# Performance work log

Hardware: AMD Instinct MI355X
Metric: run time of the kernel (lower is better)

## Reference

```python
import jax, jax.numpy as jnp
import numpy as np

NF, D, H, HD, NL, FF = 5, 64, 8, 8, 2, 128   # features, d_model, heads, head_dim, layers, ffn
NQ, QL, NC = 8, 3, 3                          # qubits, quantum layers, classes


def pos_encoding(S, d):
    pos = np.arange(S, dtype=np.float32)[:, None]
    div = np.exp(np.arange(0, d, 2, dtype=np.float32) * (-np.log(10000.0) / d))
    pe = np.zeros((S, d), np.float32)
    pe[:, 0::2] = np.sin(pos * div)
    pe[:, 1::2] = np.cos(pos * div)
    return jnp.asarray(pe)


def layernorm(x, g, b, eps=1e-5):
    m = x.mean(-1, keepdims=True)
    v = ((x - m) ** 2).mean(-1, keepdims=True)
    return (x - m) * jax.lax.rsqrt(v + eps) * g + b


def apply1q(psi, U, w):
    # psi: (2,)*NQ complex state; apply 2x2 gate U on wire w
    p = jnp.moveaxis(psi, w, 0)
    sh = p.shape
    p = (U @ p.reshape(2, -1)).reshape(sh)
    return jnp.moveaxis(p, 0, w)


def cnot(psi, c, t):
    p = jnp.moveaxis(psi, (c, t), (0, 1))
    sh = p.shape
    p = p.reshape(2, 2, -1)
    p = jnp.stack([p[0], p[1, ::-1]], 0).reshape(sh)  # flip target when control=1
    return jnp.moveaxis(p, (0, 1), (c, t))


def rx_mat(t):
    c, s = jnp.cos(t / 2), jnp.sin(t / 2)
    return jnp.stack([jnp.stack([c + 0j, -1j * s]), jnp.stack([-1j * s, c + 0j])]).astype(jnp.complex64)


def rot_mat(phi, th, om):
    # qml.Rot = RZ(om) RY(th) RZ(phi)
    c, s = jnp.cos(th / 2), jnp.sin(th / 2)
    return jnp.stack([
        jnp.stack([jnp.exp(-0.5j * (phi + om)) * c, -jnp.exp(0.5j * (phi - om)) * s]),
        jnp.stack([jnp.exp(-0.5j * (phi - om)) * s, jnp.exp(0.5j * (phi + om)) * c]),
    ]).astype(jnp.complex64)


def quantum_circuit(angles, weights):
    # angles: [NQ], weights: [QL, NQ, 3]. Circuit: QL x (AngleEmbedding(RX) + StronglyEntanglingLayer(range=1))
    psi = jnp.zeros((2,) * NQ, jnp.complex64).at[(0,) * NQ].set(1.0)
    for l in range(QL):
        for w in range(NQ):
            psi = apply1q(psi, rx_mat(angles[w]), w)
        for w in range(NQ):
            psi = apply1q(psi, rot_mat(weights[l, w, 0], weights[l, w, 1], weights[l, w, 2]), w)
        for w in range(NQ):
            psi = cnot(psi, w, (w + 1) % NQ)
    prob = jnp.abs(psi) ** 2
    zs = []
    for w in range(NC):  # <Z_w> = p(0_w) - p(1_w)
        marg = prob.sum(axis=tuple(i for i in range(NQ) if i != w))
        zs.append(marg[0] - marg[1])
    # von Neumann entropy of wires 0..3 (trace out wires 4..7), natural log
    mat = psi.reshape(16, 16)
    rho = mat @ mat.conj().T
    ev = jnp.clip(jnp.linalg.eigvalsh(rho), 1e-10, 1.0)
    ent = -jnp.sum(ev * jnp.log(ev))
    return jnp.stack(zs), ent


def setup_inputs() -> dict:
    key = jax.random.key(0)
    ks = jax.random.split(key, 30)
    sc = 0.02
    inp = {
        'x': jax.random.normal(ks[0], (16, 1024, NF), jnp.float32),
        'Wemb': sc * jax.random.normal(ks[1], (NF, D)), 'bemb': jnp.zeros((D,)),
        'Wq': sc * jax.random.normal(ks[2], (NL, D, D)), 'bq': jnp.zeros((NL, D)),
        'Wk': sc * jax.random.normal(ks[3], (NL, D, D)), 'bk': jnp.zeros((NL, D)),
        'Wv': sc * jax.random.normal(ks[4], (NL, D, D)), 'bv': jnp.zeros((NL, D)),
        'Wo': sc * jax.random.normal(ks[5], (NL, D, D)), 'bo': jnp.zeros((NL, D)),
        'ln1g': jnp.ones((NL, D)), 'ln1b': jnp.zeros((NL, D)),
        'ln2g': jnp.ones((NL, D)), 'ln2b': jnp.zeros((NL, D)),
        'Wf1': sc * jax.random.normal(ks[6], (NL, D, FF)), 'bf1': jnp.zeros((NL, FF)),
        'Wf2': sc * jax.random.normal(ks[7], (NL, FF, D)), 'bf2': jnp.zeros((NL, D)),
        'Wp1': sc * jax.random.normal(ks[8], (D, 32)), 'bp1': jnp.zeros((32,)),
        'Wp2': sc * jax.random.normal(ks[9], (32, NQ)), 'bp2': jnp.zeros((NQ,)),
        'qweights': jax.random.normal(ks[10], (QL, NQ, 3)),
    }
    return inp


def reference(x, Wemb, bemb, Wq, bq, Wk, bk, Wv, bv, Wo, bo, ln1g, ln1b, ln2g, ln2b,
              Wf1, bf1, Wf2, bf2, Wp1, bp1, Wp2, bp2, qweights):
    B, S, _ = x.shape
    h = x @ Wemb + bemb + pos_encoding(S, D)[None]  # aug + dropout are identity in eval
    scale = np.float32(1.0 / np.sqrt(HD))
    for l in range(NL):
        q = (h @ Wq[l] + bq[l]).reshape(B, S, H, HD).transpose(0, 2, 1, 3)
        k = (h @ Wk[l] + bk[l]).reshape(B, S, H, HD).transpose(0, 2, 1, 3)
        v = (h @ Wv[l] + bv[l]).reshape(B, S, H, HD).transpose(0, 2, 1, 3)
        att = jax.nn.softmax(jnp.einsum('bhsd,bhtd->bhst', q, k) * scale, axis=-1)
        o = jnp.einsum('bhst,bhtd->bhsd', att, v).transpose(0, 2, 1, 3).reshape(B, S, D)
        h = layernorm(h + o @ Wo[l] + bo[l], ln1g[l], ln1b[l])
        ff = jax.nn.relu(h @ Wf1[l] + bf1[l]) @ Wf2[l] + bf2[l]
        h = layernorm(h + ff, ln2g[l], ln2b[l])
    pooled = h.mean(1)
    feats = jax.nn.relu(pooled @ Wp1 + bp1) @ Wp2 + bp2
    angles = jnp.tanh(feats) * np.float32(np.pi)
    logits, ent = jax.vmap(quantum_circuit, in_axes=(0, None))(angles, qweights)
    return logits, ent
```

## Files before the change

### kernel.cpp

```cpp
#include <hip/hip_runtime.h>
#include <math.h>

#define BB 16
#define SS 1024
#define NF 5
#define DD 64
#define HH 8
#define HDIM 8
#define NLAYER 2
#define FFD 128
#define NQ 8
#define QLAY 3
#define NC 3
#define NSWEEP 5
#define BHS_TOT (BB * HH * SS)

typedef __fp16 hf2 __attribute__((ext_vector_type(2)));
typedef __fp16 h8  __attribute__((ext_vector_type(8)));
typedef float  f4x __attribute__((ext_vector_type(4)));

__device__ __forceinline__ int   f2i_(float x) { union { float f; int i; } u; u.f = x; return u.i; }
__device__ __forceinline__ float i2f_(int x)   { union { float f; int i; } u; u.i = x; return u.f; }

__device__ __forceinline__ float bperm_(int pa, float x) {
    return i2f_(__builtin_amdgcn_ds_bpermute(pa, f2i_(x)));
}

__device__ __forceinline__ float half32_(float x) {
#if defined(__has_builtin)
#if __has_builtin(__builtin_amdgcn_permlane32_swap)
    int xi = f2i_(x);
    auto r = __builtin_amdgcn_permlane32_swap(xi, xi, false, false);
    int r0 = (int)r[0], r1 = (int)r[1];
    return i2f_(r0 == xi ? r1 : r0);
#else
    return __shfl_xor(x, 32);
#endif
#else
    return __shfl_xor(x, 32);
#endif
}

template<int M> __device__ __forceinline__ float lx(float x) {
    if constexpr (M == 0) {
        return x;
    } else if constexpr (M == 1) {
        return i2f_(__builtin_amdgcn_update_dpp(0, f2i_(x), 0xB1, 0xF, 0xF, true));
    } else if constexpr (M == 2) {
        return i2f_(__builtin_amdgcn_update_dpp(0, f2i_(x), 0x4E, 0xF, 0xF, true));
    } else if constexpr (M == 3) {
        return i2f_(__builtin_amdgcn_update_dpp(0, f2i_(x), 0x1B, 0xF, 0xF, true));
    } else if constexpr (M < 32) {
        return i2f_(__builtin_amdgcn_ds_swizzle(f2i_(x), (M << 10) | 0x1F));
    } else {
        return lx<M & 31>(half32_(x));
    }
}

__global__ __launch_bounds__(64) void k_embed(const float* __restrict__ x,
                                              const float* __restrict__ Wemb,
                                              const float* __restrict__ bemb,
                                              float* __restrict__ h) {
    int bs = blockIdx.x;
    int s  = bs & (SS - 1);
    int d  = threadIdx.x;
    const float* xr = x + bs * NF;
    float acc = bemb[d];
#pragma unroll
    for (int f = 0; f < NF; ++f) acc += xr[f] * Wemb[f * DD + d];
    int i = d >> 1;
    float div = expf((float)(2 * i) * (-9.210340371976184f / 64.0f));
    float ang = (float)s * div;
    float pe = (d & 1) ? cosf(ang) : sinf(ang);
    h[bs * DD + d] = acc + pe;
}

__global__ __launch_bounds__(64) void k_qkv(const float* __restrict__ h,
                                            const float* __restrict__ Wq, const float* __restrict__ bq,
                                            const float* __restrict__ Wk, const float* __restrict__ bk,
                                            const float* __restrict__ Wv, const float* __restrict__ bv,
                                            hf2* __restrict__ qh, hf2* __restrict__ kh,
                                            hf2* __restrict__ vt, int l) {
    __shared__ float hrow[4][DD];
    int d   = threadIdx.x;
    int bs0 = blockIdx.x * 4;
#pragma unroll
    for (int r = 0; r < 4; ++r) hrow[r][d] = h[(bs0 + r) * DD + d];
    __syncthreads();
    const float* wq = Wq + l * DD * DD;
    const float* wk = Wk + l * DD * DD;
    const float* wv = Wv + l * DD * DD;
    float aq[4], ak[4], av[4];
    float bqv = bq[l * DD + d], bkv = bk[l * DD + d], bvv = bv[l * DD + d];
#pragma unroll
    for (int r = 0; r < 4; ++r) { aq[r] = bqv; ak[r] = bkv; av[r] = bvv; }
#pragma unroll 4
    for (int i = 0; i < DD; ++i) {
        float wqv = wq[i * DD + d], wkv = wk[i * DD + d], wvv = wv[i * DD + d];
#pragma unroll
        for (int r = 0; r < 4; ++r) {
            float hv = hrow[r][i];
            aq[r] += hv * wqv; ak[r] += hv * wkv; av[r] += hv * wvv;
        }
    }
    int hh = d >> 3, hd = d & 7;
    const float qs = 0.3535533906f;
    float aqp[4], akp[4];
#pragma unroll
    for (int r = 0; r < 4; ++r) { aqp[r] = __shfl_xor(aq[r], 1); akp[r] = __shfl_xor(ak[r], 1); }
    if ((hd & 1) == 0) {
#pragma unroll
        for (int r = 0; r < 4; ++r) {
            int bs = bs0 + r;
            int b = bs >> 10, s = bs & 1023;
            int bhs = ((b * HH + hh) << 10) | s;
            qh[bhs * 4 + (hd >> 1)] = __builtin_amdgcn_cvt_pkrtz(aq[r] * qs, aqp[r] * qs);
            kh[bhs * 4 + (hd >> 1)] = __builtin_amdgcn_cvt_pkrtz(ak[r], akp[r]);
        }
    }
    {
        int b = bs0 >> 10, s0 = bs0 & 1023;
        int vrow = (b * HH + hh) * 8 + hd;
        hf2* vp = vt + vrow * 512 + (s0 >> 1);
        vp[0] = __builtin_amdgcn_cvt_pkrtz(av[0], av[1]);
        vp[1] = __builtin_amdgcn_cvt_pkrtz(av[2], av[3]);
    }
}

__global__ __launch_bounds__(256) void k_attn(const float4* __restrict__ qh4,
                                              const float4* __restrict__ kh4,
                                              const float4* __restrict__ vt4,
                                              float* __restrict__ Ao) {
    int bh  = blockIdx.x;
    int sb  = blockIdx.y;
    int tid = threadIdx.x;
    int wv  = tid >> 6;
    int L   = tid & 63;
    int m = L & 15, quad = L >> 4;
    union U { float4 f; h8 h; };
    h8 hz = {0,0,0,0,0,0,0,0};
    h8 bQ = hz;
    if (quad == 0) { U u; u.f = qh4[(bh << 10) | (sb * 64 + wv * 16 + m)]; bQ = u.h; }
    int kmap = 8 * (m >> 2) + (m & 3);
    const float4* kbase = kh4 + (bh << 10);
    const float4* vbase = vt4 + ((bh * 8 + m) << 7);
    f4x Oacc = {0.f, 0.f, 0.f, 0.f};
    float ls = 0.f;
    for (int kc = 0; kc < 32; ++kc) {
        h8 aK0 = hz, aK1 = hz;
        if (quad == 0) {
            U u0, u1;
            u0.f = kbase[kc * 32 + kmap];
            u1.f = kbase[kc * 32 + kmap + 4];
            aK0 = u0.h; aK1 = u1.h;
        }
        f4x S0 = {0.f,0.f,0.f,0.f}, S1 = {0.f,0.f,0.f,0.f};
        S0 = __builtin_amdgcn_mfma_f32_16x16x32_f16(aK0, bQ, S0, 0, 0, 0);
        S1 = __builtin_amdgcn_mfma_f32_16x16x32_f16(aK1, bQ, S1, 0, 0, 0);
        float p0 = __expf(S0[0]), p1 = __expf(S0[1]);
        float p2 = __expf(S0[2]), p3 = __expf(S0[3]);
        float p4 = __expf(S1[0]), p5 = __expf(S1[1]);
        float p6 = __expf(S1[2]), p7 = __expf(S1[3]);
        ls += (p0 + p1 + p2 + p3) + (p4 + p5 + p6 + p7);
        hf2 c0 = __builtin_amdgcn_cvt_pkrtz(p0, p1);
        hf2 c1 = __builtin_amdgcn_cvt_pkrtz(p2, p3);
        hf2 c2 = __builtin_amdgcn_cvt_pkrtz(p4, p5);
        hf2 c3 = __builtin_amdgcn_cvt_pkrtz(p6, p7);
        h8 aP;
        aP[0] = c0[0]; aP[1] = c0[1]; aP[2] = c1[0]; aP[3] = c1[1];
        aP[4] = c2[0]; aP[5] = c2[1]; aP[6] = c3[0]; aP[7] = c3[1];
        h8 bV = hz;
        if (m < 8) {
            U uv; uv.f = vbase[kc * 4 + quad];
            bV = uv.h;
        }
        Oacc = __builtin_amdgcn_mfma_f32_16x16x32_f16(aP, bV, Oacc, 0, 0, 0);
    }
    ls += __shfl_xor(ls, 16);
    ls += __shfl_xor(ls, 32);
    float d0 = bperm_((4 * quad + 0) << 2, ls);
    float d1 = bperm_((4 * quad + 1) << 2, ls);
    float d2 = bperm_((4 * quad + 2) << 2, ls);
    float d3 = bperm_((4 * quad + 3) << 2, ls);
    if (m < 8) {
        int srow = sb * 64 + wv * 16 + quad * 4;
        int base = (((bh << 10) | srow) << 3) + m;
        Ao[base]      = Oacc[0] / d0;
        Ao[base + 8]  = Oacc[1] / d1;
        Ao[base + 16] = Oacc[2] / d2;
        Ao[base + 24] = Oacc[3] / d3;
    }
}

__global__ __launch_bounds__(128) void k_mid(const float* __restrict__ Ao,
                                             const float* __restrict__ Wo, const float* __restrict__ bo,
                                             const float* __restrict__ g1, const float* __restrict__ b1,
                                             const float* __restrict__ Wf1, const float* __restrict__ bf1,
                                             const float* __restrict__ Wf2, const float* __restrict__ bf2,
                                             const float* __restrict__ g2, const float* __restrict__ b2,
                                             float* __restrict__ h, int l) {
    __shared__ float orow[4][DD];
    __shared__ float h1s[4][DD];
    __shared__ float frow[4][FFD];
    int t    = threadIdx.x;
    int d    = t & 63;
    int half = t >> 6;
    int bs0  = blockIdx.x * 4;
    int hh = d >> 3, hd = d & 7;
    int r0 = half * 2, r1 = r0 + 1;

#pragma unroll
    for (int rr = 0; rr < 2; ++rr) {
        int r  = r0 + rr;
        int bs = bs0 + r;
        int b = bs >> 10, s = bs & 1023;
        int bhs = ((b * HH + hh) << 10) | s;
        orow[r][d] = Ao[(bhs << 3) + hd];
    }
    __syncthreads();

    {
        const float* w = Wo + l * DD * DD;
        float bias = bo[l * DD + d];
        float acc0 = bias, acc1 = bias;
#pragma unroll 4
        for (int i = 0; i < DD; ++i) {
            float wv = w[i * DD + d];
            acc0 += orow[r0][i] * wv;
            acc1 += orow[r1][i] * wv;
        }
        float gg = g1[l * DD + d], bb = b1[l * DD + d];
        float accs[2] = {acc0, acc1};
#pragma unroll
        for (int rr = 0; rr < 2; ++rr) {
            int r = r0 + rr;
            float a = accs[rr] + h[(bs0 + r) * DD + d];
            float sum = a;
            for (int off = 32; off; off >>= 1) sum += __shfl_xor(sum, off);
            float mean = sum * (1.f / 64.f);
            float dx = a - mean;
            float vs = dx * dx;
            for (int off = 32; off; off >>= 1) vs += __shfl_xor(vs, off);
            float rstd = rsqrtf(vs * (1.f / 64.f) + 1e-5f);
            h1s[r][d] = dx * rstd * gg + bb;
        }
    }
    __syncthreads();

    {
        const float* w = Wf1 + l * DD * FFD;
        float bv = bf1[l * FFD + t];
        float a0 = bv, a1 = bv, a2 = bv, a3 = bv;
#pragma unroll 4
        for (int i = 0; i < DD; ++i) {
            float wv = w[i * FFD + t];
            a0 += h1s[0][i]*wv; a1 += h1s[1][i]*wv;
            a2 += h1s[2][i]*wv; a3 += h1s[3][i]*wv;
        }
        frow[0][t] = fmaxf(a0, 0.f); frow[1][t] = fmaxf(a1, 0.f);
        frow[2][t] = fmaxf(a2, 0.f); frow[3][t] = fmaxf(a3, 0.f);
    }
    __syncthreads();

    {
        const float* w = Wf2 + l * FFD * DD;
        float bias = bf2[l * DD + d];
        float acc0 = bias, acc1 = bias;
#pragma unroll 4
        for (int i = 0; i < FFD; ++i) {
            float wv = w[i * DD + d];
            acc0 += frow[r0][i] * wv;
            acc1 += frow[r1][i] * wv;
        }
        float gg = g2[l * DD + d], bb = b2[l * DD + d];
        float accs[2] = {acc0, acc1};
#pragma unroll
        for (int rr = 0; rr < 2; ++rr) {
            int r = r0 + rr;
            float a = accs[rr] + h1s[r][d];
            float sum = a;
            for (int off = 32; off; off >>= 1) sum += __shfl_xor(sum, off);
            float mean = sum * (1.f / 64.f);
            float dx = a - mean;
            float vs = dx * dx;
            for (int off = 32; off; off >>= 1) vs += __shfl_xor(vs, off);
            float rstd = rsqrtf(vs * (1.f / 64.f) + 1e-5f);
            h[(bs0 + r) * DD + d] = dx * rstd * gg + bb;
        }
    }
}

__global__ __launch_bounds__(64) void k_pool(const float* __restrict__ h, float* __restrict__ pp) {
    int b = blockIdx.x, c = blockIdx.y, d = threadIdx.x;
    const float* hp = h + (b * SS + c * 128) * DD + d;
    float acc = 0.f;
#pragma unroll 8
    for (int s = 0; s < 128; ++s) acc += hp[s * DD];
    pp[(b * 8 + c) * DD + d] = acc;
}

__global__ __launch_bounds__(64) void k_tail(const float* __restrict__ pp,
                                             const float* __restrict__ Wp1, const float* __restrict__ bp1,
                                             const float* __restrict__ Wp2, const float* __restrict__ bp2,
                                             const float* __restrict__ qw,
                                             float* __restrict__ out) {
    __shared__ float pool_s[DD];
    __shared__ float hid[32];
    __shared__ float ang_s[NQ];
    __shared__ float ucoef[QLAY * 16][8];
    __shared__ float2 Ps2[256];
    int b = blockIdx.x; int L = threadIdx.x;
    int lb4 = L << 2;

    {
        float acc = 0.f;
#pragma unroll
        for (int c = 0; c < 8; ++c) acc += pp[(b * 8 + c) * DD + L];
        pool_s[L] = acc * (1.f / 1024.f);
    }
    __syncthreads();
    if (L < 32) {
        float a = bp1[L];
#pragma unroll 8
        for (int i = 0; i < DD; ++i) a += pool_s[i] * Wp1[i * 32 + L];
        hid[L] = fmaxf(a, 0.f);
    }
    __syncthreads();
    if (L < NQ) {
        float a = bp2[L];
#pragma unroll 8
        for (int j = 0; j < 32; ++j) a += hid[j] * Wp2[j * NQ + L];
        ang_s[L] = tanhf(a) * 3.14159265358979f;
    }
    __syncthreads();

    if (L < QLAY * 16) {
        int l = L >> 4, g8 = L & 15, w = g8 & 7;
        float u00r, u00i, u01r, u01i, u10r, u10i, u11r, u11i;
        if (g8 < 8) {
            float ha = 0.5f * ang_s[w];
            float c = __cosf(ha), s = __sinf(ha);
            u00r = c;   u00i = 0.f; u01r = 0.f; u01i = -s;
            u10r = 0.f; u10i = -s;  u11r = c;   u11i = 0.f;
        } else {
            const float* p3 = qw + (l * NQ + w) * 3;
            float phi = p3[0], th = p3[1], om = p3[2];
            float ct = __cosf(0.5f * th), st = __sinf(0.5f * th);
            float al = 0.5f * (phi + om), be = 0.5f * (phi - om);
            float ca = __cosf(al), sa = __sinf(al), cb = __cosf(be), sb = __sinf(be);
            u00r =  ct * ca; u00i = -ct * sa;
            u01r = -st * cb; u01i = -st * sb;
            u10r =  st * cb; u10i = -st * sb;
            u11r =  ct * ca; u11i =  ct * sa;
        }
        float* up = ucoef[L];
        up[0] = u00r; up[1] = u00i; up[2] = u01r; up[3] = u01i;
        up[4] = u10r; up[5] = u10i; up[6] = u11r; up[7] = u11i;
    }
    __syncthreads();

    float ar[4], ai[4];
#pragma unroll
    for (int r = 0; r < 4; ++r) { ar[r] = 0.f; ai[r] = 0.f; }
    if (L == 0) ar[0] = 1.f;

#pragma unroll 1
    for (int l = 0; l < QLAY; ++l) {
#pragma unroll 1
        for (int g8 = 0; g8 < 16; ++g8) {
            const float* up = ucoef[(l << 4) | g8];
            float u00r = up[0], u00i = up[1], u01r = up[2], u01i = up[3];
            float u10r = up[4], u10i = up[5], u11r = up[6], u11i = up[7];
            int p = 7 - (g8 & 7);
            if (p >= 6) {
#pragma unroll
                for (int pi_ = 0; pi_ < 2; ++pi_) {
                    int lo = (p == 7) ? pi_ : pi_ * 2;
                    int hi = (p == 7) ? pi_ + 2 : pi_ * 2 + 1;
                    float r0 = ar[lo], m0 = ai[lo], r1 = ar[hi], m1 = ai[hi];
                    ar[lo] = u00r*r0 - u00i*m0 + u01r*r1 - u01i*m1;
                    ai[lo] = u00r*m0 + u00i*r0 + u01r*m1 + u01i*r1;
                    ar[hi] = u10r*r0 - u10i*m0 + u11r*r1 - u11i*m1;
                    ai[hi] = u10r*m0 + u10i*r0 + u11r*m1 + u11i*r1;
                }
            } else {
                int pa  = lb4 ^ (4 << p);
                int bit = (L >> p) & 1;
                float car = bit ? u11r : u00r, cai = bit ? u11i : u00i;
                float cpr = bit ? u10r : u01r, cpi = bit ? u10i : u01i;
#pragma unroll
                for (int r = 0; r < 4; ++r) {
                    float pre = bperm_(pa, ar[r]);
                    float pim = bperm_(pa, ai[r]);
                    float nr = car*ar[r] - cai*ai[r] + cpr*pre - cpi*pim;
                    float ni = car*ai[r] + cai*ar[r] + cpr*pim + cpi*pre;
                    ar[r] = nr; ai[r] = ni;
                }
            }
        }
        { float t0=ar[2]; ar[2]=ar[3]; ar[3]=t0; t0=ai[2]; ai[2]=ai[3]; ai[3]=t0; }
        ar[1] = half32_(ar[1]); ai[1] = half32_(ai[1]);
        ar[3] = half32_(ar[3]); ai[3] = half32_(ai[3]);
#pragma unroll 1
        for (int w = 2; w <= 6; ++w) {
            int pc = 7 - w, pt = 6 - w;
            int pa = lb4 ^ (4 << pt);
            bool ctrl = (L >> pc) & 1;
#pragma unroll
            for (int r = 0; r < 4; ++r) {
                float swr = bperm_(pa, ar[r]);
                float swi = bperm_(pa, ai[r]);
                ar[r] = ctrl ? swr : ar[r];
                ai[r] = ctrl ? swi : ai[r];
            }
        }
        {
            bool ctrl = L & 1;
            float n0r = ctrl ? ar[2] : ar[0], n2r = ctrl ? ar[0] : ar[2];
            float n0i = ctrl ? ai[2] : ai[0], n2i = ctrl ? ai[0] : ai[2];
            float n1r = ctrl ? ar[3] : ar[1], n3r = ctrl ? ar[1] : ar[3];
            float n1i = ctrl ? ai[3] : ai[1], n3i = ctrl ? ai[1] : ai[3];
            ar[0]=n0r; ar[1]=n1r; ar[2]=n2r; ar[3]=n3r;
            ai[0]=n0i; ai[1]=n1i; ai[2]=n2i; ai[3]=n3i;
        }
    }

    {
        float p0 = ar[0]*ar[0]+ai[0]*ai[0];
        float p1 = ar[1]*ar[1]+ai[1]*ai[1];
        float p2 = ar[2]*ar[2]+ai[2]*ai[2];
        float p3 = ar[3]*ar[3]+ai[3]*ai[3];
        float z0 = p0 + p1 - p2 - p3;
        float z1 = p0 - p1 + p2 - p3;
        float zs = p0 + p1 + p2 + p3;
        float z2 = (L & 32) ? -zs : zs;
#pragma unroll 1
        for (int off = 1; off < 64; off <<= 1) {
            int pa = lb4 ^ (off << 2);
            z0 += bperm_(pa, z0);
            z1 += bperm_(pa, z1);
            z2 += bperm_(pa, z2);
        }
        if (L == 0) {
            out[b * NC + 0] = z0;
            out[b * NC + 1] = z1;
            out[b * NC + 2] = z2;
        }
    }

#pragma unroll
    for (int r = 0; r < 4; ++r) Ps2[(r << 6) | L] = make_float2(ar[r], ai[r]);
    __syncthreads();
    int c   = L >> 2;
    int seg = L & 3;
    float gr[4], gi[4];
#pragma unroll
    for (int j = 0; j < 4; ++j) {
        float2 t = Ps2[(seg * 4 + j) * 16 + c];
        gr[j] = t.x; gi[j] = t.y;
    }
    float alm = 0.f;
#pragma unroll
    for (int j = 0; j < 4; ++j) alm += gr[j]*gr[j] + gi[j]*gi[j];
    alm += lx<1>(alm);
    alm += lx<2>(alm);

#pragma unroll 1
    for (int sweep = 0; sweep < NSWEEP; ++sweep) {
#pragma unroll 1
        for (int m = 1; m <= 15; ++m) {
            int pa = lb4 ^ (m << 4);
            float pgr[4], pgi[4];
#pragma unroll
            for (int j = 0; j < 4; ++j) {
                pgr[j] = bperm_(pa, gr[j]);
                pgi[j] = bperm_(pa, gi[j]);
            }
            float bep = bperm_(pa, alm);
            float d = 0.f, e = 0.f;
#pragma unroll
            for (int j = 0; j < 4; ++j) {
                d += gr[j]*pgr[j] + gi[j]*pgi[j];
                e += gr[j]*pgi[j] - gi[j]*pgr[j];
            }
            d += lx<1>(d); e += lx<1>(e);
            d += lx<2>(d); e += lx<2>(e);
            float g2 = d*d + e*e;
            float cth = 1.f, sth = 0.f, cph = 1.f, sph = 0.f, gn = 0.f;
            if (g2 > 1e-26f) {
                gn = __builtin_amdgcn_sqrtf(g2);
                float ginv = __builtin_amdgcn_rcpf(gn);
                cph = d * ginv; sph = -e * ginv;
                float tau = (alm - bep) * (0.5f * ginv);
                float t = ((tau >= 0.f) ? 1.f : -1.f) *
                          __builtin_amdgcn_rcpf(fabsf(tau) + __builtin_amdgcn_sqrtf(1.f + tau*tau));
                cth = __builtin_amdgcn_rsqf(1.f + t*t);
                sth = t * cth;
            }
#pragma unroll
            for (int j = 0; j < 4; ++j) {
                float er = cph*pgr[j] - sph*pgi[j];
                float ei = cph*pgi[j] + sph*pgr[j];
                gr[j] = cth * gr[j] + sth * er;
                gi[j] = cth * gi[j] + sth * ei;
            }
            alm = cth*cth*alm + sth*sth*bep + 2.f*cth*sth*gn;
        }
    }

    float alm2 = 0.f;
#pragma unroll
    for (int j = 0; j < 4; ++j) alm2 += gr[j]*gr[j] + gi[j]*gi[j];
    alm2 += lx<1>(alm2);
    alm2 += lx<2>(alm2);

    float ev = fminf(fmaxf(alm2, 1e-10f), 1.0f);
    float term = -ev * __logf(ev);
#pragma unroll 1
    for (int off = 4; off < 64; off <<= 1) term += bperm_(lb4 ^ (off << 2), term);
    if (L == 0) out[BB * NC + b] = term;
}

extern "C" void kernel_launch(void* const* d_in, const int* in_sizes, int n_in,
                              void* d_out, int out_size, void* d_ws, size_t ws_size,
                              hipStream_t stream) {
    const float* x    = (const float*)d_in[0];
    const float* Wemb = (const float*)d_in[1];
    const float* bemb = (const float*)d_in[2];
    const float* Wq   = (const float*)d_in[3];
    const float* bq   = (const float*)d_in[4];
    const float* Wk   = (const float*)d_in[5];
    const float* bk   = (const float*)d_in[6];
    const float* Wv   = (const float*)d_in[7];
    const float* bv   = (const float*)d_in[8];
    const float* Wo   = (const float*)d_in[9];
    const float* bo   = (const float*)d_in[10];
    const float* ln1g = (const float*)d_in[11];
    const float* ln1b = (const float*)d_in[12];
    const float* ln2g = (const float*)d_in[13];
    const float* ln2b = (const float*)d_in[14];
    const float* Wf1  = (const float*)d_in[15];
    const float* bf1  = (const float*)d_in[16];
    const float* Wf2  = (const float*)d_in[17];
    const float* bf2  = (const float*)d_in[18];
    const float* Wp1  = (const float*)d_in[19];
    const float* bp1  = (const float*)d_in[20];
    const float* Wp2  = (const float*)d_in[21];
    const float* bp2  = (const float*)d_in[22];
    const float* qwts = (const float*)d_in[23];
    float* out = (float*)d_out;

    const size_t M = 1u << 20;
    float* ws   = (float*)d_ws;
    float* h    = ws;
    hf2*   qh   = (hf2*)(ws + M);
    hf2*   kh   = (hf2*)(ws + M + M / 2);
    hf2*   vt   = (hf2*)(ws + 2 * M);
    float* Ao   = ws + 2 * M + M / 2;
    float* pp   = ws + 3 * M + M / 2;

    k_embed<<<BB * SS, 64, 0, stream>>>(x, Wemb, bemb, h);
    for (int l = 0; l < NLAYER; ++l) {
        k_qkv<<<BB * SS / 4, 64, 0, stream>>>(h, Wq, bq, Wk, bk, Wv, bv, qh, kh, vt, l);
        k_attn<<<dim3(BB * HH, 16), 256, 0, stream>>>((const float4*)qh, (const float4*)kh,
                                                      (const float4*)vt, Ao);
        k_mid<<<BB * SS / 4, 128, 0, stream>>>(Ao, Wo, bo, ln1g, ln1b,
                                               Wf1, bf1, Wf2, bf2, ln2g, ln2b, h, l);
    }
    k_pool<<<dim3(BB, 8), 64, 0, stream>>>(h, pp);
    k_tail<<<BB, 64, 0, stream>>>(pp, Wp1, bp1, Wp2, bp2, qwts, out);
}
```

Baseline: 298.0 us.

## Fuse embedding into QKV, next-layer QKV into mid kernel, pooling into tail

The embedding is folded into the first QKV projection kernel. The next layer's Q/K/V projection now runs at the end of the first k_mid, working from the normalised rows held in shared memory. Pooling moves into the tail kernel, which uses 256 threads. Shuffle reductions are replaced with DPP/swizzle helpers. This cuts the launch count from 9 to 6 and removes round trips of the hidden state through global memory, at the cost of extra registers and shared memory in k_mid and a larger pooling loop per tail block.

```diff
diff --git a/kernel.cpp b/kernel.cpp
--- a/kernel.cpp
+++ b/kernel.cpp
@@ -57,41 +57,51 @@
     }
 }
 
-__global__ __launch_bounds__(64) void k_embed(const float* __restrict__ x,
-                                              const float* __restrict__ Wemb,
-                                              const float* __restrict__ bemb,
-                                              float* __restrict__ h) {
-    int bs = blockIdx.x;
-    int s  = bs & (SS - 1);
-    int d  = threadIdx.x;
-    const float* xr = x + bs * NF;
-    float acc = bemb[d];
-#pragma unroll
-    for (int f = 0; f < NF; ++f) acc += xr[f] * Wemb[f * DD + d];
-    int i = d >> 1;
-    float div = expf((float)(2 * i) * (-9.210340371976184f / 64.0f));
-    float ang = (float)s * div;
-    float pe = (d & 1) ? cosf(ang) : sinf(ang);
-    h[bs * DD + d] = acc + pe;
-}
-
-__global__ __launch_bounds__(64) void k_qkv(const float* __restrict__ h,
-                                            const float* __restrict__ Wq, const float* __restrict__ bq,
-                                            const float* __restrict__ Wk, const float* __restrict__ bk,
-                                            const float* __restrict__ Wv, const float* __restrict__ bv,
-                                            hf2* __restrict__ qh, hf2* __restrict__ kh,
-                                            hf2* __restrict__ vt, int l) {
+__device__ __forceinline__ float wsum64_(float v) {
+    v += lx<32>(v);
+    v += lx<16>(v);
+    v += lx<8>(v);
+    v += lx<4>(v);
+    v += lx<2>(v);
+    v += lx<1>(v);
+    return v;
+}
+
+__global__ __launch_bounds__(64) void k_qkv0(const float* __restrict__ x,
+                                             const float* __restrict__ Wemb,
+                                             const float* __restrict__ bemb,
+                                             const float* __restrict__ Wq, const float* __restrict__ bq,
+                                             const float* __restrict__ Wk, const float* __restrict__ bk,
+                                             const float* __restrict__ Wv, const float* __restrict__ bv,
+                                             hf2* __restrict__ qh, hf2* __restrict__ kh,
+                                             hf2* __restrict__ vt, float* __restrict__ h) {
     __shared__ float hrow[4][DD];
     int d   = threadIdx.x;
     int bs0 = blockIdx.x * 4;
-#pragma unroll
-    for (int r = 0; r < 4; ++r) hrow[r][d] = h[(bs0 + r) * DD + d];
-    __syncthreads();
-    const float* wq = Wq + l * DD * DD;
-    const float* wk = Wk + l * DD * DD;
-    const float* wv = Wv + l * DD * DD;
+    {
+        int i = d >> 1;
+        float div = expf((float)(2 * i) * (-9.210340371976184f / 64.0f));
+#pragma unroll
+        for (int r = 0; r < 4; ++r) {
+            int bs = bs0 + r;
+            int s  = bs & (SS - 1);
+            const float* xr = x + bs * NF;
+            float acc = bemb[d];
+#pragma unroll
+            for (int f = 0; f < NF; ++f) acc += xr[f] * Wemb[f * DD + d];
+            float ang = (float)s * div;
+            float pe = (d & 1) ? cosf(ang) : sinf(ang);
+            float hv = acc + pe;
+            hrow[r][d] = hv;
+            h[bs * DD + d] = hv;
+        }
+    }
+    __syncthreads();
+    const float* wq = Wq;
+    const float* wk = Wk;
+    const float* wv = Wv;
     float aq[4], ak[4], av[4];
-    float bqv = bq[l * DD + d], bkv = bk[l * DD + d], bvv = bv[l * DD + d];
+    float bqv = bq[d], bkv = bk[d], bvv = bv[d];
 #pragma unroll
     for (int r = 0; r < 4; ++r) { aq[r] = bqv; ak[r] = bkv; av[r] = bvv; }
 #pragma unroll 4
@@ -107,7 +117,7 @@
     const float qs = 0.3535533906f;
     float aqp[4], akp[4];
 #pragma unroll
-    for (int r = 0; r < 4; ++r) { aqp[r] = __shfl_xor(aq[r], 1); akp[r] = __shfl_xor(ak[r], 1); }
+    for (int r = 0; r < 4; ++r) { aqp[r] = lx<1>(aq[r]); akp[r] = lx<1>(ak[r]); }
     if ((hd & 1) == 0) {
 #pragma unroll
         for (int r = 0; r < 4; ++r) {
@@ -143,7 +153,7 @@
     if (quad == 0) { U u; u.f = qh4[(bh << 10) | (sb * 64 + wv * 16 + m)]; bQ = u.h; }
     int kmap = 8 * (m >> 2) + (m & 3);
     const float4* kbase = kh4 + (bh << 10);
-    const float4* vbase = vt4 + ((bh * 8 + m) << 7);
+    const float4* vbase = vt4 + ((bh * 8 + (m & 7)) << 7);
     f4x Oacc = {0.f, 0.f, 0.f, 0.f};
     float ls = 0.f;
     for (int kc = 0; kc < 32; ++kc) {
@@ -176,8 +186,8 @@
         }
         Oacc = __builtin_amdgcn_mfma_f32_16x16x32_f16(aP, bV, Oacc, 0, 0, 0);
     }
-    ls += __shfl_xor(ls, 16);
-    ls += __shfl_xor(ls, 32);
+    ls += lx<16>(ls);
+    ls += lx<32>(ls);
     float d0 = bperm_((4 * quad + 0) << 2, ls);
     float d1 = bperm_((4 * quad + 1) << 2, ls);
     float d2 = bperm_((4 * quad + 2) << 2, ls);
@@ -198,10 +208,16 @@
                                              const float* __restrict__ Wf1, const float* __restrict__ bf1,
                                              const float* __restrict__ Wf2, const float* __restrict__ bf2,
                                              const float* __restrict__ g2, const float* __restrict__ b2,
-                                             float* __restrict__ h, int l) {
+                                             float* __restrict__ h, int l, int fuse,
+                                             const float* __restrict__ Wq, const float* __restrict__ bq,
+                                             const float* __restrict__ Wk, const float* __restrict__ bk,
+                                             const float* __restrict__ Wv, const float* __restrict__ bv,
+                                             hf2* __restrict__ qh, hf2* __restrict__ kh,
+                                             hf2* __restrict__ vt) {
     __shared__ float orow[4][DD];
     __shared__ float h1s[4][DD];
     __shared__ float frow[4][FFD];
+    __shared__ float hfin[4][DD];
     int t    = threadIdx.x;
     int d    = t & 63;
     int half = t >> 6;
@@ -235,12 +251,10 @@
         for (int rr = 0; rr < 2; ++rr) {
             int r = r0 + rr;
             float a = accs[rr] + h[(bs0 + r) * DD + d];
-            float sum = a;
-            for (int off = 32; off; off >>= 1) sum += __shfl_xor(sum, off);
+            float sum = wsum64_(a);
             float mean = sum * (1.f / 64.f);
             float dx = a - mean;
-            float vs = dx * dx;
-            for (int off = 32; off; off >>= 1) vs += __shfl_xor(vs, off);
+            float vs = wsum64_(dx * dx);
             float rstd = rsqrtf(vs * (1.f / 64.f) + 1e-5f);
             h1s[r][d] = dx * rstd * gg + bb;
         }
@@ -249,8 +263,8 @@
 
     {
         const float* w = Wf1 + l * DD * FFD;
-        float bv = bf1[l * FFD + t];
-        float a0 = bv, a1 = bv, a2 = bv, a3 = bv;
+        float bv_ = bf1[l * FFD + t];
+        float a0 = bv_, a1 = bv_, a2 = bv_, a3 = bv_;
 #pragma unroll 4
         for (int i = 0; i < DD; ++i) {
             float wv = w[i * FFD + t];
@@ -278,64 +292,114 @@
         for (int rr = 0; rr < 2; ++rr) {
             int r = r0 + rr;
             float a = accs[rr] + h1s[r][d];
-            float sum = a;
-            for (int off = 32; off; off >>= 1) sum += __shfl_xor(sum, off);
+            float sum = wsum64_(a);
             float mean = sum * (1.f / 64.f);
             float dx = a - mean;
-            float vs = dx * dx;
-            for (int off = 32; off; off >>= 1) vs += __shfl_xor(vs, off);
+            float vs = wsum64_(dx * dx);
             float rstd = rsqrtf(vs * (1.f / 64.f) + 1e-5f);
-            h[(bs0 + r) * DD + d] = dx * rstd * gg + bb;
-        }
-    }
-}
-
-__global__ __launch_bounds__(64) void k_pool(const float* __restrict__ h, float* __restrict__ pp) {
-    int b = blockIdx.x, c = blockIdx.y, d = threadIdx.x;
-    const float* hp = h + (b * SS + c * 128) * DD + d;
-    float acc = 0.f;
-#pragma unroll 8
-    for (int s = 0; s < 128; ++s) acc += hp[s * DD];
-    pp[(b * 8 + c) * DD + d] = acc;
-}
-
-__global__ __launch_bounds__(64) void k_tail(const float* __restrict__ pp,
-                                             const float* __restrict__ Wp1, const float* __restrict__ bp1,
-                                             const float* __restrict__ Wp2, const float* __restrict__ bp2,
-                                             const float* __restrict__ qw,
-                                             float* __restrict__ out) {
+            float hv = dx * rstd * gg + bb;
+            hfin[r][d] = hv;
+            h[(bs0 + r) * DD + d] = hv;
+        }
+    }
+
+    if (!fuse) return;
+
+    __syncthreads();
+    const int l1 = l + 1;
+    if (t < 64) {
+        const float* wq = Wq + l1 * DD * DD;
+        const float* wk = Wk + l1 * DD * DD;
+        float aq[4], ak[4];
+        float bqv = bq[l1 * DD + d], bkv = bk[l1 * DD + d];
+#pragma unroll
+        for (int r = 0; r < 4; ++r) { aq[r] = bqv; ak[r] = bkv; }
+#pragma unroll 4
+        for (int i = 0; i < DD; ++i) {
+            float wqv = wq[i * DD + d], wkv = wk[i * DD + d];
+#pragma unroll
+            for (int r = 0; r < 4; ++r) {
+                float hv = hfin[r][i];
+                aq[r] += hv * wqv; ak[r] += hv * wkv;
+            }
+        }
+        const float qs = 0.3535533906f;
+        float aqp[4], akp[4];
+#pragma unroll
+        for (int r = 0; r < 4; ++r) { aqp[r] = lx<1>(aq[r]); akp[r] = lx<1>(ak[r]); }
+        if ((hd & 1) == 0) {
+#pragma unroll
+            for (int r = 0; r < 4; ++r) {
+                int bs = bs0 + r;
+                int b = bs >> 10, s = bs & 1023;
+                int bhs = ((b * HH + hh) << 10) | s;
+                qh[bhs * 4 + (hd >> 1)] = __builtin_amdgcn_cvt_pkrtz(aq[r] * qs, aqp[r] * qs);
+                kh[bhs * 4 + (hd >> 1)] = __builtin_amdgcn_cvt_pkrtz(ak[r], akp[r]);
+            }
+        }
+    } else {
+        const float* wv = Wv + l1 * DD * DD;
+        float av[4];
+        float bvv = bv[l1 * DD + d];
+#pragma unroll
+        for (int r = 0; r < 4; ++r) av[r] = bvv;
+#pragma unroll 4
+        for (int i = 0; i < DD; ++i) {
+            float wvv = wv[i * DD + d];
+#pragma unroll
+            for (int r = 0; r < 4; ++r) av[r] += hfin[r][i] * wvv;
+        }
+        int b = bs0 >> 10, s0 = bs0 & 1023;
+        int vrow = (b * HH + hh) * 8 + hd;
+        hf2* vp = vt + vrow * 512 + (s0 >> 1);
+        vp[0] = __builtin_amdgcn_cvt_pkrtz(av[0], av[1]);
+        vp[1] = __builtin_amdgcn_cvt_pkrtz(av[2], av[3]);
+    }
+}
+
+__global__ __launch_bounds__(256) void k_tail(const float* __restrict__ h,
+                                              const float* __restrict__ Wp1, const float* __restrict__ bp1,
+                                              const float* __restrict__ Wp2, const float* __restrict__ bp2,
+                                              const float* __restrict__ qw,
+                                              float* __restrict__ out) {
+    __shared__ float part[4][DD];
     __shared__ float pool_s[DD];
     __shared__ float hid[32];
     __shared__ float ang_s[NQ];
     __shared__ float ucoef[QLAY * 16][8];
     __shared__ float2 Ps2[256];
-    int b = blockIdx.x; int L = threadIdx.x;
-    int lb4 = L << 2;
+    int b = blockIdx.x; int t = threadIdx.x;
+    int L = t;
+    int lb4 = (t & 63) << 2;
 
     {
+        int d = t & 63, ch = t >> 6;
+        const float* hp = h + (b * SS + ch * 256) * DD + d;
         float acc = 0.f;
-#pragma unroll
-        for (int c = 0; c < 8; ++c) acc += pp[(b * 8 + c) * DD + L];
-        pool_s[L] = acc * (1.f / 1024.f);
-    }
-    __syncthreads();
-    if (L < 32) {
-        float a = bp1[L];
 #pragma unroll 8
-        for (int i = 0; i < DD; ++i) a += pool_s[i] * Wp1[i * 32 + L];
-        hid[L] = fmaxf(a, 0.f);
-    }
-    __syncthreads();
-    if (L < NQ) {
-        float a = bp2[L];
+        for (int s = 0; s < 256; ++s) acc += hp[s * DD];
+        part[ch][d] = acc;
+    }
+    __syncthreads();
+    if (t < 64) pool_s[t] = (part[0][t] + part[1][t] + part[2][t] + part[3][t]) * (1.f / 1024.f);
+    __syncthreads();
+    if (t < 32) {
+        float a = bp1[t];
 #pragma unroll 8
-        for (int j = 0; j < 32; ++j) a += hid[j] * Wp2[j * NQ + L];
-        ang_s[L] = tanhf(a) * 3.14159265358979f;
-    }
-    __syncthreads();
-
-    if (L < QLAY * 16) {
-        int l = L >> 4, g8 = L & 15, w = g8 & 7;
+        for (int i = 0; i < DD; ++i) a += pool_s[i] * Wp1[i * 32 + t];
+        hid[t] = fmaxf(a, 0.f);
+    }
+    __syncthreads();
+    if (t < NQ) {
+        float a = bp2[t];
+#pragma unroll 8
+        for (int j = 0; j < 32; ++j) a += hid[j] * Wp2[j * NQ + t];
+        ang_s[t] = tanhf(a) * 3.14159265358979f;
+    }
+    __syncthreads();
+
+    if (t < QLAY * 16) {
+        int l = t >> 4, g8 = t & 15, w = g8 & 7;
         float u00r, u00i, u01r, u01i, u10r, u10i, u11r, u11i;
         if (g8 < 8) {
             float ha = 0.5f * ang_s[w];
@@ -353,7 +417,7 @@
             u10r =  st * cb; u10i = -st * sb;
             u11r =  ct * ca; u11i =  ct * sa;
         }
-        float* up = ucoef[L];
+        float* up = ucoef[t];
         up[0] = u00r; up[1] = u00i; up[2] = u01r; up[3] = u01i;
         up[4] = u10r; up[5] = u10i; up[6] = u11r; up[7] = u11i;
     }
@@ -364,161 +428,166 @@
     for (int r = 0; r < 4; ++r) { ar[r] = 0.f; ai[r] = 0.f; }
     if (L == 0) ar[0] = 1.f;
 
+    if (t < 64) {
 #pragma unroll 1
-    for (int l = 0; l < QLAY; ++l) {
+        for (int l = 0; l < QLAY; ++l) {
 #pragma unroll 1
-        for (int g8 = 0; g8 < 16; ++g8) {
-            const float* up = ucoef[(l << 4) | g8];
-            float u00r = up[0], u00i = up[1], u01r = up[2], u01i = up[3];
-            float u10r = up[4], u10i = up[5], u11r = up[6], u11i = up[7];
-            int p = 7 - (g8 & 7);
-            if (p >= 6) {
-#pragma unroll
-                for (int pi_ = 0; pi_ < 2; ++pi_) {
-                    int lo = (p == 7) ? pi_ : pi_ * 2;
-                    int hi = (p == 7) ? pi_ + 2 : pi_ * 2 + 1;
-                    float r0 = ar[lo], m0 = ai[lo], r1 = ar[hi], m1 = ai[hi];
-                    ar[lo] = u00r*r0 - u00i*m0 + u01r*r1 - u01i*m1;
-                    ai[lo] = u00r*m0 + u00i*r0 + u01r*m1 + u01i*r1;
-                    ar[hi] = u10r*r0 - u10i*m0 + u11r*r1 - u11i*m1;
-                    ai[hi] = u10r*m0 + u10i*r0 + u11r*m1 + u11i*r1;
+            for (int g8 = 0; g8 < 16; ++g8) {
+                const float* up = ucoef[(l << 4) | g8];
+                float u00r = up[0], u00i = up[1], u01r = up[2], u01i = up[3];
+                float u10r = up[4], u10i = up[5], u11r = up[6], u11i = up[7];
+                int p = 7 - (g8 & 7);
+                if (p >= 6) {
+#pragma unroll
+                    for (int pi_ = 0; pi_ < 2; ++pi_) {
+                        int lo = (p == 7) ? pi_ : pi_ * 2;
+                        int hi = (p == 7) ? pi_ + 2 : pi_ * 2 + 1;
+                        float r0 = ar[lo], m0 = ai[lo], r1 = ar[hi], m1 = ai[hi];
+                        ar[lo] = u00r*r0 - u00i*m0 + u01r*r1 - u01i*m1;
+                        ai[lo] = u00r*m0 + u00i*r0 + u01r*m1 + u01i*r1;
+                        ar[hi] = u10r*r0 - u10i*m0 + u11r*r1 - u11i*m1;
+                        ai[hi] = u10r*m0 + u10i*r0 + u11r*m1 + u11i*r1;
+                    }
+                } else {
+                    int pa  = lb4 ^ (4 << p);
+                    int bit = (L >> p) & 1;
+                    float car = bit ? u11r : u00r, cai = bit ? u11i : u00i;
+                    float cpr = bit ? u10r : u01r, cpi = bit ? u10i : u01i;
+#pragma unroll
+                    for (int r = 0; r < 4; ++r) {
+                        float pre = bperm_(pa, ar[r]);
+                        float pim = bperm_(pa, ai[r]);
+                        float nr = car*ar[r] - cai*ai[r] + cpr*pre - cpi*pim;
+                        float ni = car*ai[r] + cai*ar[r] + cpr*pim + cpi*pre;
+                        ar[r] = nr; ai[r] = ni;
+                    }
                 }
-            } else {
-                int pa  = lb4 ^ (4 << p);
-                int bit = (L >> p) & 1;
-                float car = bit ? u11r : u00r, cai = bit ? u11i : u00i;
-                float cpr = bit ? u10r : u01r, cpi = bit ? u10i : u01i;
+            }
+            { float t0=ar[2]; ar[2]=ar[3]; ar[3]=t0; t0=ai[2]; ai[2]=ai[3]; ai[3]=t0; }
+            ar[1] = half32_(ar[1]); ai[1] = half32_(ai[1]);
+            ar[3] = half32_(ar[3]); ai[3] = half32_(ai[3]);
+#pragma unroll 1
+            for (int w = 2; w <= 6; ++w) {
+                int pc = 7 - w, pt = 6 - w;
+                int pa = lb4 ^ (4 << pt);
+                bool ctrl = (L >> pc) & 1;
 #pragma unroll
                 for (int r = 0; r < 4; ++r) {
-                    float pre = bperm_(pa, ar[r]);
-                    float pim = bperm_(pa, ai[r]);
-                    float nr = car*ar[r] - cai*ai[r] + cpr*pre - cpi*pim;
-                    float ni = car*ai[r] + cai*ar[r] + cpr*pim + cpi*pre;
-                    ar[r] = nr; ai[r] = ni;
+                    float swr = bperm_(pa, ar[r]);
+                    float swi = bperm_(pa, ai[r]);
+                    ar[r] = ctrl ? swr : ar[r];
+                    ai[r] = ctrl ? swi : ai[r];
                 }
             }
-        }
-        { float t0=ar[2]; ar[2]=ar[3]; ar[3]=t0; t0=ai[2]; ai[2]=ai[3]; ai[3]=t0; }
-        ar[1] = half32_(ar[1]); ai[1] = half32_(ai[1]);
-        ar[3] = half32_(ar[3]); ai[3] = half32_(ai[3]);
+            {
+                bool ctrl = L & 1;
+                float n0r = ctrl ? ar[2] : ar[0], n2r = ctrl ? ar[0] : ar[2];
+                float n0i = ctrl ? ai[2] : ai[0], n2i = ctrl ? ai[0] : ai[2];
+                float n1r = ctrl ? ar[3] : ar[1], n3r = ctrl ? ar[1] : ar[3];
+                float n1i = ctrl ? ai[3] : ai[1], n3i = ctrl ? ai[1] : ai[3];
+                ar[0]=n0r; ar[1]=n1r; ar[2]=n2r; ar[3]=n3r;
+                ai[0]=n0i; ai[1]=n1i; ai[2]=n2i; ai[3]=n3i;
+            }
+        }
+
+        {
+            float p0 = ar[0]*ar[0]+ai[0]*ai[0];
+            float p1 = ar[1]*ar[1]+ai[1]*ai[1];
+            float p2 = ar[2]*ar[2]+ai[2]*ai[2];
+            float p3 = ar[3]*ar[3]+ai[3]*ai[3];
+            float z0 = p0 + p1 - p2 - p3;
+            float z1 = p0 - p1 + p2 - p3;
+            float zs = p0 + p1 + p2 + p3;
+            float z2 = (L & 32) ? -zs : zs;
 #pragma unroll 1
-        for (int w = 2; w <= 6; ++w) {
-            int pc = 7 - w, pt = 6 - w;
-            int pa = lb4 ^ (4 << pt);
-            bool ctrl = (L >> pc) & 1;
-#pragma unroll
-            for (int r = 0; r < 4; ++r) {
-                float swr = bperm_(pa, ar[r]);
-                float swi = bperm_(pa, ai[r]);
-                ar[r] = ctrl ? swr : ar[r];
-                ai[r] = ctrl ? swi : ai[r];
-            }
-        }
-        {
-            bool ctrl = L & 1;
-            float n0r = ctrl ? ar[2] : ar[0], n2r = ctrl ? ar[0] : ar[2];
-            float n0i = ctrl ? ai[2] : ai[0], n2i = ctrl ? ai[0] : ai[2];
-            float n1r = ctrl ? ar[3] : ar[1], n3r = ctrl ? ar[1] : ar[3];
-            float n1i = ctrl ? ai[3] : ai[1], n3i = ctrl ? ai[1] : ai[3];
-            ar[0]=n0r; ar[1]=n1r; ar[2]=n2r; ar[3]=n3r;
-            ai[0]=n0i; ai[1]=n1i; ai[2]=n2i; ai[3]=n3i;
-        }
-    }
-
-    {
-        float p0 = ar[0]*ar[0]+ai[0]*ai[0];
-        float p1 = ar[1]*ar[1]+ai[1]*ai[1];
-        float p2 = ar[2]*ar[2]+ai[2]*ai[2];
-        float p3 = ar[3]*ar[3]+ai[3]*ai[3];
-        float z0 = p0 + p1 - p2 - p3;
-        float z1 = p0 - p1 + p2 - p3;
-        float zs = p0 + p1 + p2 + p3;
-        float z2 = (L & 32) ? -zs : zs;
+            for (int off = 1; off < 64; off <<= 1) {
+                int pa = lb4 ^ (off << 2);
+                z0 += bperm_(pa, z0);
+                z1 += bperm_(pa, z1);
+                z2 += bperm_(pa, z2);
+            }
+            if (L == 0) {
+                out[b * NC + 0] = z0;
+                out[b * NC + 1] = z1;
+                out[b * NC + 2] = z2;
+            }
+        }
+
+#pragma unroll
+        for (int r = 0; r < 4; ++r) Ps2[(r << 6) | L] = make_float2(ar[r], ai[r]);
+    }
+    __syncthreads();
+
+    if (t < 64) {
+        int c   = L >> 2;
+        int seg = L & 3;
+        float gr[4], gi[4];
+#pragma unroll
+        for (int j = 0; j < 4; ++j) {
+            float2 tv = Ps2[(seg * 4 + j) * 16 + c];
+            gr[j] = tv.x; gi[j] = tv.y;
+        }
+        float alm = 0.f;
+#pragma unroll
+        for (int j = 0; j < 4; ++j) alm += gr[j]*gr[j] + gi[j]*gi[j];
+        alm += lx<1>(alm);
+        alm += lx<2>(alm);
+
 #pragma unroll 1
-        for (int off = 1; off < 64; off <<= 1) {
-            int pa = lb4 ^ (off << 2);
-            z0 += bperm_(pa, z0);
-            z1 += bperm_(pa, z1);
-            z2 += bperm_(pa, z2);
-        }
-        if (L == 0) {
-            out[b * NC + 0] = z0;
-            out[b * NC + 1] = z1;
-            out[b * NC + 2] = z2;
-        }
-    }
-
-#pragma unroll
-    for (int r = 0; r < 4; ++r) Ps2[(r << 6) | L] = make_float2(ar[r], ai[r]);
-    __syncthreads();
-    int c   = L >> 2;
-    int seg = L & 3;
-    float gr[4], gi[4];
-#pragma unroll
-    for (int j = 0; j < 4; ++j) {
-        float2 t = Ps2[(seg * 4 + j) * 16 + c];
-        gr[j] = t.x; gi[j] = t.y;
-    }
-    float alm = 0.f;
-#pragma unroll
-    for (int j = 0; j < 4; ++j) alm += gr[j]*gr[j] + gi[j]*gi[j];
-    alm += lx<1>(alm);
-    alm += lx<2>(alm);
-
+        for (int sweep = 0; sweep < NSWEEP; ++sweep) {
 #pragma unroll 1
-    for (int sweep = 0; sweep < NSWEEP; ++sweep) {
+            for (int m = 1; m <= 15; ++m) {
+                int pa = lb4 ^ (m << 4);
+                float pgr[4], pgi[4];
+#pragma unroll
+                for (int j = 0; j < 4; ++j) {
+                    pgr[j] = bperm_(pa, gr[j]);
+                    pgi[j] = bperm_(pa, gi[j]);
+                }
+                float bep = bperm_(pa, alm);
+                float d = 0.f, e = 0.f;
+#pragma unroll
+                for (int j = 0; j < 4; ++j) {
+                    d += gr[j]*pgr[j] + gi[j]*pgi[j];
+                    e += gr[j]*pgi[j] - gi[j]*pgr[j];
+                }
+                d += lx<1>(d); e += lx<1>(e);
+                d += lx<2>(d); e += lx<2>(e);
+                float g2 = d*d + e*e;
+                float cth = 1.f, sth = 0.f, cph = 1.f, sph = 0.f, gn = 0.f;
+                if (g2 > 1e-26f) {
+                    gn = __builtin_amdgcn_sqrtf(g2);
+                    float ginv = __builtin_amdgcn_rcpf(gn);
+                    cph = d * ginv; sph = -e * ginv;
+                    float tau = (alm - bep) * (0.5f * ginv);
+                    float tt = ((tau >= 0.f) ? 1.f : -1.f) *
+                               __builtin_amdgcn_rcpf(fabsf(tau) + __builtin_amdgcn_sqrtf(1.f + tau*tau));
+                    cth = __builtin_amdgcn_rsqf(1.f + tt*tt);
+                    sth = tt * cth;
+                }
+#pragma unroll
+                for (int j = 0; j < 4; ++j) {
+                    float er = cph*pgr[j] - sph*pgi[j];
+                    float ei = cph*pgi[j] + sph*pgr[j];
+                    gr[j] = cth * gr[j] + sth * er;
+                    gi[j] = cth * gi[j] + sth * ei;
+                }
+                alm = cth*cth*alm + sth*sth*bep + 2.f*cth*sth*gn;
+            }
+        }
+
+        float alm2 = 0.f;
+#pragma unroll
+        for (int j = 0; j < 4; ++j) alm2 += gr[j]*gr[j] + gi[j]*gi[j];
+        alm2 += lx<1>(alm2);
+        alm2 += lx<2>(alm2);
+
+        float ev = fminf(fmaxf(alm2, 1e-10f), 1.0f);
+        float term = -ev * __logf(ev);
 #pragma unroll 1
-        for (int m = 1; m <= 15; ++m) {
-            int pa = lb4 ^ (m << 4);
-            float pgr[4], pgi[4];
-#pragma unroll
-            for (int j = 0; j < 4; ++j) {
-                pgr[j] = bperm_(pa, gr[j]);
-                pgi[j] = bperm_(pa, gi[j]);
-            }
-            float bep = bperm_(pa, alm);
-            float d = 0.f, e = 0.f;
-#pragma unroll
-            for (int j = 0; j < 4; ++j) {
-                d += gr[j]*pgr[j] + gi[j]*pgi[j];
-                e += gr[j]*pgi[j] - gi[j]*pgr[j];
-            }
-            d += lx<1>(d); e += lx<1>(e);
-            d += lx<2>(d); e += lx<2>(e);
-            float g2 = d*d + e*e;
-            float cth = 1.f, sth = 0.f, cph = 1.f, sph = 0.f, gn = 0.f;
-            if (g2 > 1e-26f) {
-                gn = __builtin_amdgcn_sqrtf(g2);
-                float ginv = __builtin_amdgcn_rcpf(gn);
-                cph = d * ginv; sph = -e * ginv;
-                float tau = (alm - bep) * (0.5f * ginv);
-                float t = ((tau >= 0.f) ? 1.f : -1.f) *
-                          __builtin_amdgcn_rcpf(fabsf(tau) + __builtin_amdgcn_sqrtf(1.f + tau*tau));
-                cth = __builtin_amdgcn_rsqf(1.f + t*t);
-                sth = t * cth;
-            }
-#pragma unroll
-            for (int j = 0; j < 4; ++j) {
-                float er = cph*pgr[j] - sph*pgi[j];
-                float ei = cph*pgi[j] + sph*pgr[j];
-                gr[j] = cth * gr[j] + sth * er;
-                gi[j] = cth * gi[j] + sth * ei;
-            }
-            alm = cth*cth*alm + sth*sth*bep + 2.f*cth*sth*gn;
-        }
-    }
-
-    float alm2 = 0.f;
-#pragma unroll
-    for (int j = 0; j < 4; ++j) alm2 += gr[j]*gr[j] + gi[j]*gi[j];
-    alm2 += lx<1>(alm2);
-    alm2 += lx<2>(alm2);
-
-    float ev = fminf(fmaxf(alm2, 1e-10f), 1.0f);
-    float term = -ev * __logf(ev);
-#pragma unroll 1
-    for (int off = 4; off < 64; off <<= 1) term += bperm_(lb4 ^ (off << 2), term);
-    if (L == 0) out[BB * NC + b] = term;
+        for (int off = 4; off < 64; off <<= 1) term += bperm_(lb4 ^ (off << 2), term);
+        if (L == 0) out[BB * NC + b] = term;
+    }
 }
 
 extern "C" void kernel_launch(void* const* d_in, const int* in_sizes, int n_in,
@@ -557,16 +626,18 @@
     hf2*   kh   = (hf2*)(ws + M + M / 2);
     hf2*   vt   = (hf2*)(ws + 2 * M);
     float* Ao   = ws + 2 * M + M / 2;
-    float* pp   = ws + 3 * M + M / 2;
-
-    k_embed<<<BB * SS, 64, 0, stream>>>(x, Wemb, bemb, h);
-    for (int l = 0; l < NLAYER; ++l) {
-        k_qkv<<<BB * SS / 4, 64, 0, stream>>>(h, Wq, bq, Wk, bk, Wv, bv, qh, kh, vt, l);
-        k_attn<<<dim3(BB * HH, 16), 256, 0, stream>>>((const float4*)qh, (const float4*)kh,
-                                                      (const float4*)vt, Ao);
-        k_mid<<<BB * SS / 4, 128, 0, stream>>>(Ao, Wo, bo, ln1g, ln1b,
-                                               Wf1, bf1, Wf2, bf2, ln2g, ln2b, h, l);
-    }
-    k_pool<<<dim3(BB, 8), 64, 0, stream>>>(h, pp);
-    k_tail<<<BB, 64, 0, stream>>>(pp, Wp1, bp1, Wp2, bp2, qwts, out);
-}
+
+    k_qkv0<<<BB * SS / 4, 64, 0, stream>>>(x, Wemb, bemb, Wq, bq, Wk, bk, Wv, bv,
+                                           qh, kh, vt, h);
+    k_attn<<<dim3(BB * HH, 16), 256, 0, stream>>>((const float4*)qh, (const float4*)kh,
+                                                  (const float4*)vt, Ao);
+    k_mid<<<BB * SS / 4, 128, 0, stream>>>(Ao, Wo, bo, ln1g, ln1b,
+                                           Wf1, bf1, Wf2, bf2, ln2g, ln2b, h, 0, 1,
+                                           Wq, bq, Wk, bk, Wv, bv, qh, kh, vt);
+    k_attn<<<dim3(BB * HH, 16), 256, 0, stream>>>((const float4*)qh, (const float4*)kh,
+                                                  (const float4*)vt, Ao);
+    k_mid<<<BB * SS / 4, 128, 0, stream>>>(Ao, Wo, bo, ln1g, ln1b,
+                                           Wf1, bf1, Wf2, bf2, ln2g, ln2b, h, 1, 0,
+                                           Wq, bq, Wk, bk, Wv, bv, qh, kh, vt);
+    k_tail<<<BB, 256, 0, stream>>>(h, Wp1, bp1, Wp2, bp2, qwts, out);
+}
```

New measurement: 287.7 us. -3.4%, faster.
